# Kernel optimization log

Measured on AMD Instinct MI355X. Metric: run time of the kernel, lower is better.

## Reference

```python
import jax, jax.numpy as jnp
import numpy as np

B, N, H, L, E, OUT = 32, 128, 128, 3, 65536, 128
AV, BV = 128, 16  # atom / bond feature vocab sizes
NEG = -1e9


def setup_inputs() -> dict:
    key = jax.random.key(0)
    ks = jax.random.split(key, 20)
    x = jax.random.randint(ks[0], (B * N, 9), 0, AV)          # OGB atom features
    edge_attr = jax.random.randint(ks[1], (E, 3), 0, BV)      # OGB bond features
    # within-graph random edges (PyG requires edges not to cross graphs)
    g = jax.random.randint(ks[2], (E,), 0, B)
    src = jax.random.randint(ks[3], (E,), 0, N)
    dst = jax.random.randint(ks[4], (E,), 0, N)
    edge_index = jnp.stack([g * N + src, g * N + dst])        # [2, E] global node ids
    batch_idx = jnp.repeat(jnp.arange(B), N)                  # equal-size graphs
    s = 0.05
    w = lambda k, *shape: jax.random.normal(k, shape, dtype=jnp.float32) * s
    return {
        "x": x, "edge_attr": edge_attr, "edge_index": edge_index, "batch_idx": batch_idx,
        "atom_emb": w(ks[5], 9, AV, H), "bond_emb": w(ks[6], 3, BV, H),
        "Wm1": w(ks[7], L, 2 * H, H), "bm1": jnp.zeros((L, H), jnp.float32),
        "Wm2": w(ks[8], L, 2 * H, H), "bm2": jnp.zeros((L, H), jnp.float32),
        "We": w(ks[9], L, H, H), "be": jnp.zeros((L, H), jnp.float32),
        "Wg": w(ks[10], L, H, H), "bg": jnp.zeros((L, H), jnp.float32),
        "Wp1": w(ks[11], L, H, H), "bp1": jnp.zeros((L, H), jnp.float32),
        "Wp2": w(ks[12], L, H, H), "bp2": jnp.zeros((L, H), jnp.float32),
        "Wo1": w(ks[13], L, 2 * H, H), "bo1": jnp.zeros((L, H), jnp.float32),
        "Wo2": w(ks[14], L, H, H), "bo2": jnp.zeros((L, H), jnp.float32),
        "ln_s": jnp.ones((L, H), jnp.float32), "ln_b": jnp.zeros((L, H), jnp.float32),
        "Wh1": w(ks[15], H, H), "bh1": jnp.zeros((H,), jnp.float32),
        "Wh2": w(ks[16], H, OUT), "bh2": jnp.zeros((OUT,), jnp.float32),
    }


def reference(x, edge_attr, edge_index, batch_idx, atom_emb, bond_emb,
              Wm1, bm1, Wm2, bm2, We, be, Wg, bg, Wp1, bp1, Wp2, bp2,
              Wo1, bo1, Wo2, bo2, ln_s, ln_b, Wh1, bh1, Wh2, bh2):
    # AtomEncoder / BondEncoder: sum of per-column embeddings
    node_fts = jnp.sum(atom_emb[jnp.arange(9), x], axis=1)        # [B*N, H]
    edge_fts = jnp.sum(bond_emb[jnp.arange(3), edge_attr], axis=1)  # [E, H]
    # to_dense_batch with equal-size graphs == reshape; mask all-True
    node_fts = node_fts.reshape(B, N, H)
    # to_dense_adj: scatter-add edge list into dense [B, N, N] (+features)
    g = edge_index[0] // N
    s_loc = edge_index[0] % N
    d_loc = edge_index[1] % N
    adj = jnp.zeros((B, N, N), jnp.float32).at[g, s_loc, d_loc].add(1.0)
    edge_dense = jnp.zeros((B, N, N, H), jnp.float32).at[g, s_loc, d_loc].add(edge_fts)
    graph_fts = jnp.zeros((B, H), jnp.float32)
    hidden = jnp.zeros_like(node_fts)
    adj_mask = (adj > 0)[..., None]                               # [B, Ns, Nr, 1]
    for l in range(L):  # CLRS-style MPNN layers
        z = jnp.concatenate([node_fts, hidden], axis=-1)          # [B, N, 2H]
        m1 = z @ Wm1[l] + bm1[l]
        m2 = z @ Wm2[l] + bm2[l]
        me = edge_dense @ We[l] + be[l]
        mg = graph_fts @ Wg[l] + bg[l]
        msgs = m1[:, :, None, :] + m2[:, None, :, :] + me + mg[:, None, None, :]
        msgs = jax.nn.relu(msgs)
        msgs = jax.nn.relu(msgs @ Wp1[l] + bp1[l]) @ Wp2[l] + bp2[l]  # msgs MLP [H,H]
        msgs = jnp.max(jnp.where(adj_mask, msgs, NEG), axis=1)   # masked max over senders
        h = jax.nn.relu(z @ Wo1[l] + bo1[l] + msgs @ Wo2[l] + bo2[l])
        mu = h.mean(-1, keepdims=True)
        var = ((h - mu) ** 2).mean(-1, keepdims=True)
        hidden = (h - mu) / jnp.sqrt(var + 1e-5) * ln_s[l] + ln_b[l]
    # masked mean pool (mask is all-True here) + prediction MLP
    graph_emb = hidden.mean(axis=1)                               # [B, H]
    return jax.nn.relu(graph_emb @ Wh1 + bh1) @ Wh2 + bh2         # [B, OUT]
```

## Files before the change

### kernel.cpp

```cpp
#include <hip/hip_runtime.h>
#include <hip/hip_bf16.h>

#define NB_ 32
#define LL_ 3
#define EE_ 65536
#define NODES_ 4096
#define SLOTS_ 524288
#define NEGV -1e9f

typedef _Float16 f16x8 __attribute__((ext_vector_type(8)));
typedef float f32x4 __attribute__((ext_vector_type(4)));

__device__ __forceinline__ unsigned fkey(float f) {
  unsigned b = __float_as_uint(f);
  unsigned m = ((int)b >> 31) | 0x80000000u;
  return b ^ m;
}
__device__ __forceinline__ float funkey(unsigned k) {
  unsigned xm = (k & 0x80000000u) ? 0x80000000u : 0xFFFFFFFFu;
  return __uint_as_float(k ^ xm);
}

__global__ __launch_bounds__(256) void k_pro(const int* __restrict__ x,
    const float* __restrict__ atom_emb, _Float16* __restrict__ zh,
    const float* __restrict__ Wp1, const float* __restrict__ Wp2,
    const float* __restrict__ Wm1, const float* __restrict__ Wm2,
    const float* __restrict__ Wo1, const float* __restrict__ Wo2,
    _Float16* __restrict__ Whf,
    const float* __restrict__ bond_emb, const float* __restrict__ We,
    _Float16* __restrict__ bembWeh,
    const int* __restrict__ ei, int* __restrict__ cnt, int* __restrict__ erank) {
  int blk = blockIdx.x, tid = threadIdx.x;
  if (blk < 2048) {
    int v = blk * 2 + (tid >> 7), t = tid & 127;
    float acc = 0.f;
#pragma unroll
    for (int c = 0; c < 9; c++) {
      int xv = x[v * 9 + c];
      acc += atom_emb[(c * 128 + xv) * 128 + t];
    }
    zh[v * 256 + t] = (_Float16)acc;
    zh[v * 256 + 128 + t] = (_Float16)0.f;
  } else if (blk < 2264) {
    int gid = (blk - 2048) * 256 + tid;
    int lane = gid & 63;
    int llo = lane & 15, lhi = lane >> 4;
    const float* W; int col, kbase;
    if (gid < 12288) {
      int mat = gid >> 11, pos = gid & 2047;
      int fr = pos >> 6; int ct = fr >> 2, kt = fr & 3;
      int lyr = mat >> 1, which = mat & 1;
      W = (which ? Wp2 : Wp1) + lyr * 16384;
      col = ct * 16 + llo; kbase = kt * 32 + lhi * 8;
    } else if (gid < 36864) {
      int q = gid - 12288;
      int lyr = q >> 13, r = q & 8191;
      int fr = r >> 6; int ct = fr >> 3, kt = fr & 7;
      col = ct * 16 + llo; kbase = kt * 32 + lhi * 8;
      if (col < 128) { W = Wm1 + lyr * 32768; }
      else { W = Wm2 + lyr * 32768; col -= 128; }
    } else {
      int q = gid - 36864;
      int lyr = q / 6144, r = q % 6144;
      int fr = r >> 6; int ct = fr / 12, kt = fr % 12;
      col = ct * 16 + llo; kbase = kt * 32 + lhi * 8;
      if (kbase < 256) { W = Wo1 + lyr * 32768; }
      else { W = Wo2 + lyr * 16384; kbase -= 256; }
    }
    f16x8 h;
#pragma unroll
    for (int e = 0; e < 8; e++) h[e] = (_Float16)W[(kbase + e) * 128 + col];
    ((f16x8*)Whf)[gid] = h;
  } else if (blk < 2336) {
    __shared__ float row[2][128];
    int rid = (blk - 2264) * 2 + (tid >> 7);
    int half = tid >> 7, c = tid & 127;
    int l = rid / 48, rr = rid % 48;
    row[half][c] = bond_emb[rr * 128 + c];
    __syncthreads();
    const float* W = We + l * 16384;
    float acc = 0.f;
    for (int k = 0; k < 128; k += 4) {
      acc += row[half][k] * W[k * 128 + c] +
             row[half][k + 1] * W[(k + 1) * 128 + c] +
             row[half][k + 2] * W[(k + 2) * 128 + c] +
             row[half][k + 3] * W[(k + 3) * 128 + c];
    }
    bembWeh[(l * 48 + rr) * 128 + c] = (_Float16)acc;
  } else {
    int e = (blk - 2336) * 256 + tid;
    int s = ei[e], d = ei[EE_ + e];
    int g = s >> 7, i = s & 127, j = d & 127;
    int slot = ((g << 7) + j) * 128 + i;
    erank[e] = atomicAdd(&cnt[slot], 1);
  }
}

__global__ __launch_bounds__(256) void k_scanA(const int* __restrict__ cnt,
    int* __restrict__ basep, int* __restrict__ pairbase,
    int* __restrict__ bsumA, int* __restrict__ bsumF) {
  __shared__ int sA[256], sF[256];
  int t = threadIdx.x, gid = blockIdx.x * 256 + t;
  int v = cnt[gid];
  int f = v > 0 ? 1 : 0;
  sA[t] = v; sF[t] = f; __syncthreads();
  for (int st = 1; st < 256; st <<= 1) {
    int aA = sA[t], aF = sF[t];
    int bA = (t >= st) ? sA[t - st] : 0;
    int bF = (t >= st) ? sF[t - st] : 0;
    __syncthreads();
    sA[t] = aA + bA; sF[t] = aF + bF;
    __syncthreads();
  }
  basep[gid] = sA[t] - v;
  pairbase[gid] = sF[t] - f;
  if (t == 255) { bsumA[blockIdx.x] = sA[255]; bsumF[blockIdx.x] = sF[255]; }
}

__global__ __launch_bounds__(256) void k_scan2d(int* __restrict__ bsumA,
                                                int* __restrict__ bsumF) {
  int* bsum = blockIdx.x ? bsumF : bsumA;
  __shared__ int s[256];
  int t = threadIdx.x;
  int v[8]; int tot = 0;
#pragma unroll
  for (int q = 0; q < 8; q++) { v[q] = bsum[t * 8 + q]; tot += v[q]; }
  s[t] = tot; __syncthreads();
  for (int st = 1; st < 256; st <<= 1) {
    int a = s[t]; int b = (t >= st) ? s[t - st] : 0;
    __syncthreads(); s[t] = a + b; __syncthreads();
  }
  int run = s[t] - tot;
#pragma unroll
  for (int q = 0; q < 8; q++) { int tmp = v[q]; bsum[t * 8 + q] = run; run += tmp; }
}

__global__ __launch_bounds__(256) void k_scanBS(const int* __restrict__ cnt,
    const int* __restrict__ basep, const int* __restrict__ pairbase,
    const int* __restrict__ bsumA, const int* __restrict__ bsumF,
    int* __restrict__ pair_total, int* __restrict__ pair_slot,
    int* __restrict__ pair_off, int* __restrict__ pair_cnt,
    const int* __restrict__ ei, const int* __restrict__ erank,
    int* __restrict__ sorted_e) {
  int blk = blockIdx.x, tid = threadIdx.x;
  if (blk < 2048) {
    int gid = blk * 256 + tid;
    int b = basep[gid] + bsumA[gid >> 8];
    int pb = pairbase[gid] + bsumF[gid >> 8];
    int c = cnt[gid];
    if (c > 0) {
      pair_slot[pb] = gid;
      pair_off[pb] = b;
      pair_cnt[pb] = c;
    }
    if (gid == SLOTS_ - 1) pair_total[0] = pb + (c > 0 ? 1 : 0);
  } else {
    int e = (blk - 2048) * 256 + tid;
    int s = ei[e], d = ei[EE_ + e];
    int g = s >> 7, i = s & 127, j = d & 127;
    int slot = ((g << 7) + j) * 128 + i;
    int pos = basep[slot] + bsumA[slot >> 8] + erank[e];
    sorted_e[pos] = e;
  }
}

__global__ __launch_bounds__(256, 4) void k_m12(const _Float16* __restrict__ zh,
    const _Float16* __restrict__ Whf, const float* __restrict__ bm1,
    const float* __restrict__ bm2, _Float16* __restrict__ mm,
    unsigned* __restrict__ msgs_u, int l) {
  int tid = threadIdx.x;
  {
    int g0 = blockIdx.x * 256 + tid;
    unsigned kneg = fkey(NEGV);
    msgs_u[g0] = kneg;
    msgs_u[g0 + 262144] = kneg;
  }
  int wv = tid >> 6, l64 = tid & 63;
  int llo = l64 & 15, lhi = l64 >> 4;
  int tile = blockIdx.x >> 2;
  int ct = (blockIdx.x & 3) * 4 + wv;
  int row = tile * 16 + llo;
  f16x8 a[8];
#pragma unroll
  for (int kt = 0; kt < 8; kt++)
    a[kt] = *(const f16x8*)(zh + row * 256 + kt * 32 + lhi * 8);
  const f16x8* Bf = (const f16x8*)Whf + 12288 + l * 8192;
  int col = ct * 16 + llo;
  float bv = (col < 128) ? bm1[l * 128 + col] : bm2[l * 128 + col - 128];
  f32x4 acc = {bv, bv, bv, bv};
#pragma unroll
  for (int kt = 0; kt < 8; kt++)
    acc = __builtin_amdgcn_mfma_f32_16x16x32_f16(a[kt], Bf[(ct * 8 + kt) * 64 + l64], acc, 0, 0, 0);
#pragma unroll
  for (int reg = 0; reg < 4; reg++)
    mm[(tile * 16 + lhi * 4 + reg) * 256 + col] = (_Float16)acc[reg];
}

__global__ __launch_bounds__(256, 4) void k_pairs(
    const _Float16* __restrict__ mm,
    const int* __restrict__ pair_slot, const int* __restrict__ pair_off,
    const int* __restrict__ pair_cnt, const int* __restrict__ pair_total,
    const int* __restrict__ sorted_e, const int* __restrict__ edge_attr,
    const _Float16* __restrict__ bembWeh,
    const float* __restrict__ be, const float* __restrict__ bg,
    const _Float16* __restrict__ Whf,
    const float* __restrict__ bp1, const float* __restrict__ bp2,
    unsigned* __restrict__ msgs_u, int l) {
  __shared__ int s_slot[64], s_off[64], s_cnt[64], s_lrow[64];
  __shared__ int s_scan[64];
  __shared__ int s_rid[16];
  __shared__ int s_nrecv;
  __shared__ unsigned Lmax[16 * 128];
  __shared__ _Float16 Uh[64 * 128];
  int P = pair_total[0];
  int pid0 = blockIdx.x * 64;
  if (pid0 >= P) return;
  int tid = threadIdx.x;
  {
    unsigned kneg = fkey(NEGV);
#pragma unroll
    for (int q = 0; q < 8; q++) Lmax[tid + q * 256] = kneg;
  }
  if (tid < 64) {
    int pid = pid0 + tid;
    bool va = pid < P;
    s_slot[tid] = va ? pair_slot[pid] : -1;
    s_off[tid] = va ? pair_off[pid] : 0;
    s_cnt[tid] = va ? pair_cnt[pid] : 0;
  }
  __syncthreads();
  if (tid < 64) {
    int slot = s_slot[tid];
    int r = slot >= 0 ? (slot >> 7) : -1;
    int pr = (tid == 0) ? -2 : (s_slot[tid - 1] >= 0 ? (s_slot[tid - 1] >> 7) : -1);
    s_scan[tid] = (slot >= 0 && r != pr) ? 1 : 0;
  }
  __syncthreads();
  for (int st = 1; st < 64; st <<= 1) {
    int a = 0, b = 0;
    if (tid < 64) { a = s_scan[tid]; b = (tid >= st) ? s_scan[tid - st] : 0; }
    __syncthreads();
    if (tid < 64) s_scan[tid] = a + b;
    __syncthreads();
  }
  if (tid < 64) {
    int slot = s_slot[tid];
    int lr = s_scan[tid] - 1;
    s_lrow[tid] = lr;
    int r = slot >= 0 ? (slot >> 7) : -1;
    int pr = (tid == 0) ? -2 : (s_slot[tid - 1] >= 0 ? (s_slot[tid - 1] >> 7) : -1);
    if (slot >= 0 && r != pr && lr < 16) s_rid[lr] = r;
    if (tid == 63) s_nrecv = s_scan[63];
  }
  __syncthreads();

  int l64 = tid & 63, wv = tid >> 6;
  int llo = l64 & 15, lhi = l64 >> 4;
  int p = wv * 16 + llo;
  int slot = s_slot[p];
  float t32[4][8];
  if (slot >= 0) {
    int rr = slot >> 7, i = slot & 127, g = slot >> 14;
    int sn = (g << 7) + i;
#pragma unroll
    for (int kt = 0; kt < 4; kt++) {
      int c0 = kt * 32 + lhi * 8;
      f16x8 v1 = *(const f16x8*)(mm + sn * 256 + c0);
      f16x8 v2 = *(const f16x8*)(mm + rr * 256 + 128 + c0);
      float4 e0 = *(const float4*)(be + l * 128 + c0);
      float4 e1 = *(const float4*)(be + l * 128 + c0 + 4);
      float4 g0 = *(const float4*)(bg + l * 128 + c0);
      float4 g1 = *(const float4*)(bg + l * 128 + c0 + 4);
      t32[kt][0] = (float)v1[0] + (float)v2[0] + e0.x + g0.x;
      t32[kt][1] = (float)v1[1] + (float)v2[1] + e0.y + g0.y;
      t32[kt][2] = (float)v1[2] + (float)v2[2] + e0.z + g0.z;
      t32[kt][3] = (float)v1[3] + (float)v2[3] + e0.w + g0.w;
      t32[kt][4] = (float)v1[4] + (float)v2[4] + e1.x + g1.x;
      t32[kt][5] = (float)v1[5] + (float)v2[5] + e1.y + g1.y;
      t32[kt][6] = (float)v1[6] + (float)v2[6] + e1.z + g1.z;
      t32[kt][7] = (float)v1[7] + (float)v2[7] + e1.w + g1.w;
    }
    int off = s_off[p], cn = s_cnt[p];
    for (int d = 0; d < cn; d++) {
      int eid = sorted_e[off + d];
      int a0 = edge_attr[eid * 3], a1 = edge_attr[eid * 3 + 1],
          a2 = edge_attr[eid * 3 + 2];
      const _Float16* r0 = bembWeh + (l * 48 + a0) * 128;
      const _Float16* r1 = bembWeh + (l * 48 + 16 + a1) * 128;
      const _Float16* r2 = bembWeh + (l * 48 + 32 + a2) * 128;
#pragma unroll
      for (int kt = 0; kt < 4; kt++) {
        int c0 = kt * 32 + lhi * 8;
        f16x8 x0 = *(const f16x8*)(r0 + c0);
        f16x8 x1 = *(const f16x8*)(r1 + c0);
        f16x8 x2 = *(const f16x8*)(r2 + c0);
#pragma unroll
        for (int e = 0; e < 8; e++)
          t32[kt][e] += (float)x0[e] + (float)x1[e] + (float)x2[e];
      }
    }
  } else {
#pragma unroll
    for (int kt = 0; kt < 4; kt++)
#pragma unroll
      for (int e = 0; e < 8; e++) t32[kt][e] = 0.f;
  }
  f16x8 a[4];
#pragma unroll
  for (int kt = 0; kt < 4; kt++)
#pragma unroll
    for (int e = 0; e < 8; e++) a[kt][e] = (_Float16)fmaxf(t32[kt][e], 0.f);

  const f16x8* W1f = (const f16x8*)Whf + (l * 2) * 2048;
  const f16x8* W2f = (const f16x8*)Whf + (l * 2 + 1) * 2048;
#pragma unroll
  for (int ct = 0; ct < 8; ct++) {
    int col = ct * 16 + llo;
    float b1 = bp1[l * 128 + col];
    f32x4 acc = {b1, b1, b1, b1};
#pragma unroll
    for (int kt = 0; kt < 4; kt++)
      acc = __builtin_amdgcn_mfma_f32_16x16x32_f16(a[kt], W1f[(ct * 4 + kt) * 64 + l64], acc, 0, 0, 0);
#pragma unroll
    for (int reg = 0; reg < 4; reg++) {
      int wrow = wv * 16 + lhi * 4 + reg;
      int sg = (2 * ct + (llo >> 3)) ^ (wrow & 15);
      Uh[wrow * 128 + sg * 8 + (llo & 7)] = (_Float16)fmaxf(acc[reg], 0.f);
    }
  }
  __syncthreads();
  f16x8 a2[4];
  int arow = wv * 16 + llo;
#pragma unroll
  for (int kt = 0; kt < 4; kt++) {
    int sg = (kt * 4 + lhi) ^ (arow & 15);
    a2[kt] = *(const f16x8*)(Uh + arow * 128 + sg * 8);
  }
#pragma unroll
  for (int ct = 0; ct < 8; ct++) {
    int col = ct * 16 + llo;
    float b2 = bp2[l * 128 + col];
    f32x4 acc = {b2, b2, b2, b2};
#pragma unroll
    for (int kt = 0; kt < 4; kt++)
      acc = __builtin_amdgcn_mfma_f32_16x16x32_f16(a2[kt], W2f[(ct * 4 + kt) * 64 + l64], acc, 0, 0, 0);
    int prev_lr = -2, prev_rr = -1; float run = 0.f;
#pragma unroll
    for (int reg = 0; reg < 4; reg++) {
      int prow = wv * 16 + lhi * 4 + reg;
      int slot2 = s_slot[prow];
      if (slot2 < 0) continue;
      int lr = s_lrow[prow];
      float v = acc[reg];
      if (lr == prev_lr) {
        run = fmaxf(run, v);
      } else {
        if (prev_lr >= 0) {
          if (prev_lr < 16) atomicMax(&Lmax[prev_lr * 128 + col], fkey(run));
          else atomicMax(&msgs_u[prev_rr * 128 + col], fkey(run));
        }
        prev_lr = lr; prev_rr = slot2 >> 7; run = v;
      }
    }
    if (prev_lr >= 0) {
      if (prev_lr < 16) atomicMax(&Lmax[prev_lr * 128 + col], fkey(run));
      else atomicMax(&msgs_u[prev_rr * 128 + col], fkey(run));
    }
  }
  __syncthreads();
  int nr = s_nrecv; if (nr > 16) nr = 16;
  for (int base = 0; base < nr; base += 2) {
    int lr = base + (tid >> 7);
    int col = tid & 127;
    if (lr < nr)
      atomicMax(&msgs_u[s_rid[lr] * 128 + col], Lmax[lr * 128 + col]);
  }
}

__global__ __launch_bounds__(512, 2) void k_out_ln(_Float16* __restrict__ zh,
    const unsigned* __restrict__ msgs_u, const _Float16* __restrict__ Whf,
    const float* __restrict__ bo1, const float* __restrict__ bo2,
    const float* __restrict__ ln_s, const float* __restrict__ ln_b, int l) {
  __shared__ float sumA[8][16];
  __shared__ float muS[16], rsS[16];
  int tid = threadIdx.x;
  int wv = tid >> 6, l64 = tid & 63;
  int llo = l64 & 15, lhi = l64 >> 4;
  int row = blockIdx.x * 16 + llo;
  f16x8 a[12];
#pragma unroll
  for (int kt = 0; kt < 8; kt++)
    a[kt] = *(const f16x8*)(zh + row * 256 + kt * 32 + lhi * 8);
#pragma unroll
  for (int kt = 8; kt < 12; kt++) {
    int k0 = (kt - 8) * 32 + lhi * 8;
    f16x8 h;
#pragma unroll
    for (int e = 0; e < 8; e++) {
      float v = funkey(msgs_u[row * 128 + k0 + e]);
      v = fmaxf(fminf(v, 60000.f), -60000.f);
      h[e] = (_Float16)v;
    }
    a[kt] = h;
  }
  const f16x8* Bf = (const f16x8*)Whf + 36864 + l * 6144;
  int ct = wv, col = ct * 16 + llo;
  float bv = bo1[l * 128 + col] + bo2[l * 128 + col];
  f32x4 acc = {bv, bv, bv, bv};
#pragma unroll
  for (int kt = 0; kt < 12; kt++)
    acc = __builtin_amdgcn_mfma_f32_16x16x32_f16(a[kt], Bf[(ct * 12 + kt) * 64 + l64], acc, 0, 0, 0);
  float h[4];
#pragma unroll
  for (int reg = 0; reg < 4; reg++) h[reg] = fmaxf(acc[reg], 0.f);
#pragma unroll
  for (int reg = 0; reg < 4; reg++) {
    float s = h[reg];
    s += __shfl_xor(s, 1, 64); s += __shfl_xor(s, 2, 64);
    s += __shfl_xor(s, 4, 64); s += __shfl_xor(s, 8, 64);
    if (llo == 0) sumA[wv][lhi * 4 + reg] = s;
  }
  __syncthreads();
  if (tid < 16) {
    float s = 0.f;
#pragma unroll
    for (int w = 0; w < 8; w++) s += sumA[w][tid];
    muS[tid] = s * (1.f / 128.f);
  }
  __syncthreads();
#pragma unroll
  for (int reg = 0; reg < 4; reg++) {
    float d = h[reg] - muS[lhi * 4 + reg];
    float s = d * d;
    s += __shfl_xor(s, 1, 64); s += __shfl_xor(s, 2, 64);
    s += __shfl_xor(s, 4, 64); s += __shfl_xor(s, 8, 64);
    if (llo == 0) sumA[wv][lhi * 4 + reg] = s;
  }
  __syncthreads();
  if (tid < 16) {
    float s = 0.f;
#pragma unroll
    for (int w = 0; w < 8; w++) s += sumA[w][tid];
    rsS[tid] = rsqrtf(s * (1.f / 128.f) + 1e-5f);
  }
  __syncthreads();
  float sc = ln_s[l * 128 + col], bb = ln_b[l * 128 + col];
#pragma unroll
  for (int reg = 0; reg < 4; reg++) {
    int rr = lhi * 4 + reg;
    int wrow = blockIdx.x * 16 + rr;
    zh[wrow * 256 + 128 + col] =
        (_Float16)((h[reg] - muS[rr]) * rsS[rr] * sc + bb);
  }
}

__global__ __launch_bounds__(128) void k_head(const _Float16* __restrict__ zh,
    const float* __restrict__ Wh1, const float* __restrict__ bh1,
    const float* __restrict__ Wh2, const float* __restrict__ bh2,
    float* __restrict__ out) {
  __shared__ float ge[128], p1[128];
  int b = blockIdx.x, t = threadIdx.x;
  float s = 0.f;
  for (int n = 0; n < 128; n++) s += (float)zh[(b * 128 + n) * 256 + 128 + t];
  ge[t] = s * (1.f / 128.f);
  __syncthreads();
  float a = bh1[t];
  for (int k = 0; k < 128; k++) a += ge[k] * Wh1[k * 128 + t];
  p1[t] = fmaxf(a, 0.f);
  __syncthreads();
  float o = bh2[t];
  for (int k = 0; k < 128; k++) o += p1[k] * Wh2[k * 128 + t];
  out[b * 128 + t] = o;
}

extern "C" void kernel_launch(void* const* d_in, const int* in_sizes, int n_in,
                              void* d_out, int out_size, void* d_ws, size_t ws_size,
                              hipStream_t stream) {
  const int* x          = (const int*)d_in[0];
  const int* edge_attr  = (const int*)d_in[1];
  const int* edge_index = (const int*)d_in[2];
  const float* atom_emb = (const float*)d_in[4];
  const float* bond_emb = (const float*)d_in[5];
  const float* Wm1 = (const float*)d_in[6];
  const float* bm1 = (const float*)d_in[7];
  const float* Wm2 = (const float*)d_in[8];
  const float* bm2 = (const float*)d_in[9];
  const float* We  = (const float*)d_in[10];
  const float* be  = (const float*)d_in[11];
  const float* bg  = (const float*)d_in[13];
  const float* Wp1 = (const float*)d_in[14];
  const float* bp1 = (const float*)d_in[15];
  const float* Wp2 = (const float*)d_in[16];
  const float* bp2 = (const float*)d_in[17];
  const float* Wo1 = (const float*)d_in[18];
  const float* bo1 = (const float*)d_in[19];
  const float* Wo2 = (const float*)d_in[20];
  const float* bo2 = (const float*)d_in[21];
  const float* ln_s = (const float*)d_in[22];
  const float* ln_b = (const float*)d_in[23];
  const float* Wh1 = (const float*)d_in[24];
  const float* bh1 = (const float*)d_in[25];
  const float* Wh2 = (const float*)d_in[26];
  const float* bh2 = (const float*)d_in[27];
  float* out = (float*)d_out;

  int* cnt       = (int*)d_ws;
  int* basep     = cnt + SLOTS_;
  int* pairbase  = basep + SLOTS_;
  int* bsumA     = pairbase + SLOTS_;
  int* bsumF     = bsumA + 2048;
  int* pair_tot  = bsumF + 2048;
  int* erank     = pair_tot + 16;
  int* sorted_e  = erank + EE_;
  int* pair_slot = sorted_e + EE_;
  int* pair_off  = pair_slot + EE_;
  int* pair_cnt  = pair_off + EE_;
  unsigned* msgs_u = (unsigned*)(pair_cnt + EE_);
  _Float16* zh   = (_Float16*)(msgs_u + SLOTS_);
  _Float16* mm   = zh + NODES_ * 256;
  _Float16* bembWeh = mm + NODES_ * 256;
  _Float16* Whf  = bembWeh + 3 * 48 * 128;

  hipMemsetAsync(cnt, 0, SLOTS_ * sizeof(int), stream);

  k_pro<<<2592, 256, 0, stream>>>(x, atom_emb, zh, Wp1, Wp2, Wm1, Wm2, Wo1, Wo2,
                                  Whf, bond_emb, We, bembWeh, edge_index, cnt,
                                  erank);
  k_scanA<<<SLOTS_ / 256, 256, 0, stream>>>(cnt, basep, pairbase, bsumA, bsumF);
  k_scan2d<<<2, 256, 0, stream>>>(bsumA, bsumF);
  k_scanBS<<<2304, 256, 0, stream>>>(cnt, basep, pairbase, bsumA, bsumF,
                                     pair_tot, pair_slot, pair_off, pair_cnt,
                                     edge_index, erank, sorted_e);

  for (int l = 0; l < LL_; l++) {
    k_m12<<<1024, 256, 0, stream>>>(zh, Whf, bm1, bm2, mm, msgs_u, l);
    k_pairs<<<1024, 256, 0, stream>>>(mm, pair_slot, pair_off, pair_cnt,
                                      pair_tot, sorted_e, edge_attr, bembWeh,
                                      be, bg, Whf, bp1, bp2, msgs_u, l);
    k_out_ln<<<NODES_ / 16, 512, 0, stream>>>(zh, msgs_u, Whf, bo1, bo2,
                                              ln_s, ln_b, l);
  }
  k_head<<<NB_, 128, 0, stream>>>(zh, Wh1, bh1, Wh2, bh2, out);
}
```

Before: 267.8 us.

## Precompute per-pair edge projections once and fuse out-LN with next layer m12

```diff
diff --git a/kernel.cpp b/kernel.cpp
--- a/kernel.cpp
+++ b/kernel.cpp
@@ -26,9 +26,7 @@
     const float* __restrict__ Wp1, const float* __restrict__ Wp2,
     const float* __restrict__ Wm1, const float* __restrict__ Wm2,
     const float* __restrict__ Wo1, const float* __restrict__ Wo2,
-    _Float16* __restrict__ Whf,
-    const float* __restrict__ bond_emb, const float* __restrict__ We,
-    _Float16* __restrict__ bembWeh,
+    const float* __restrict__ We, _Float16* __restrict__ Whf,
     const int* __restrict__ ei, int* __restrict__ cnt, int* __restrict__ erank) {
   int blk = blockIdx.x, tid = threadIdx.x;
   if (blk < 2048) {
@@ -41,7 +39,7 @@
     }
     zh[v * 256 + t] = (_Float16)acc;
     zh[v * 256 + 128 + t] = (_Float16)0.f;
-  } else if (blk < 2264) {
+  } else if (blk < 2288) {
     int gid = (blk - 2048) * 256 + tid;
     int lane = gid & 63;
     int llo = lane & 15, lhi = lane >> 4;
@@ -59,36 +57,26 @@
       col = ct * 16 + llo; kbase = kt * 32 + lhi * 8;
       if (col < 128) { W = Wm1 + lyr * 32768; }
       else { W = Wm2 + lyr * 32768; col -= 128; }
-    } else {
+    } else if (gid < 55296) {
       int q = gid - 36864;
       int lyr = q / 6144, r = q % 6144;
       int fr = r >> 6; int ct = fr / 12, kt = fr % 12;
       col = ct * 16 + llo; kbase = kt * 32 + lhi * 8;
       if (kbase < 256) { W = Wo1 + lyr * 32768; }
       else { W = Wo2 + lyr * 16384; kbase -= 256; }
+    } else {
+      int q = gid - 55296;
+      int lyr = q >> 11, r = q & 2047;
+      int fr = r >> 6; int ct = fr >> 2, kt = fr & 3;
+      W = We + lyr * 16384;
+      col = ct * 16 + llo; kbase = kt * 32 + lhi * 8;
     }
     f16x8 h;
 #pragma unroll
     for (int e = 0; e < 8; e++) h[e] = (_Float16)W[(kbase + e) * 128 + col];
     ((f16x8*)Whf)[gid] = h;
-  } else if (blk < 2336) {
-    __shared__ float row[2][128];
-    int rid = (blk - 2264) * 2 + (tid >> 7);
-    int half = tid >> 7, c = tid & 127;
-    int l = rid / 48, rr = rid % 48;
-    row[half][c] = bond_emb[rr * 128 + c];
-    __syncthreads();
-    const float* W = We + l * 16384;
-    float acc = 0.f;
-    for (int k = 0; k < 128; k += 4) {
-      acc += row[half][k] * W[k * 128 + c] +
-             row[half][k + 1] * W[(k + 1) * 128 + c] +
-             row[half][k + 2] * W[(k + 2) * 128 + c] +
-             row[half][k + 3] * W[(k + 3) * 128 + c];
-    }
-    bembWeh[(l * 48 + rr) * 128 + c] = (_Float16)acc;
   } else {
-    int e = (blk - 2336) * 256 + tid;
+    int e = (blk - 2288) * 256 + tid;
     int s = ei[e], d = ei[EE_ + e];
     int g = s >> 7, i = s & 127, j = d & 127;
     int slot = ((g << 7) + j) * 128 + i;
@@ -164,6 +152,74 @@
   }
 }
 
+__global__ __launch_bounds__(256, 4) void k_epre(
+    const int* __restrict__ pair_off, const int* __restrict__ pair_cnt,
+    const int* __restrict__ pair_total, const int* __restrict__ sorted_e,
+    const int* __restrict__ edge_attr, const float* __restrict__ bond_emb,
+    const _Float16* __restrict__ Whf, _Float16* __restrict__ eWeh) {
+  __shared__ int s_off[64], s_cnt[64];
+  int P = pair_total[0];
+  int pid0 = blockIdx.x * 64;
+  if (pid0 >= P) return;
+  int tid = threadIdx.x;
+  if (tid < 64) {
+    int pid = pid0 + tid;
+    bool va = pid < P;
+    s_off[tid] = va ? pair_off[pid] : 0;
+    s_cnt[tid] = va ? pair_cnt[pid] : 0;
+  }
+  __syncthreads();
+  int l64 = tid & 63, wv = tid >> 6;
+  int llo = l64 & 15, lhi = l64 >> 4;
+  int p = wv * 16 + llo;
+  float eb[4][8];
+#pragma unroll
+  for (int kt = 0; kt < 4; kt++)
+#pragma unroll
+    for (int e = 0; e < 8; e++) eb[kt][e] = 0.f;
+  int off = s_off[p], cn = s_cnt[p];
+  for (int d = 0; d < cn; d++) {
+    int eid = sorted_e[off + d];
+    int a0 = edge_attr[eid * 3], a1 = edge_attr[eid * 3 + 1],
+        a2 = edge_attr[eid * 3 + 2];
+    const float* r0 = bond_emb + a0 * 128;
+    const float* r1 = bond_emb + (16 + a1) * 128;
+    const float* r2 = bond_emb + (32 + a2) * 128;
+#pragma unroll
+    for (int kt = 0; kt < 4; kt++) {
+      int c0 = kt * 32 + lhi * 8;
+      float4 xa = *(const float4*)(r0 + c0), xb = *(const float4*)(r0 + c0 + 4);
+      float4 ya = *(const float4*)(r1 + c0), yb = *(const float4*)(r1 + c0 + 4);
+      float4 za = *(const float4*)(r2 + c0), zb = *(const float4*)(r2 + c0 + 4);
+      eb[kt][0] += xa.x + ya.x + za.x; eb[kt][1] += xa.y + ya.y + za.y;
+      eb[kt][2] += xa.z + ya.z + za.z; eb[kt][3] += xa.w + ya.w + za.w;
+      eb[kt][4] += xb.x + yb.x + zb.x; eb[kt][5] += xb.y + yb.y + zb.y;
+      eb[kt][6] += xb.z + yb.z + zb.z; eb[kt][7] += xb.w + yb.w + zb.w;
+    }
+  }
+  f16x8 a[4];
+#pragma unroll
+  for (int kt = 0; kt < 4; kt++)
+#pragma unroll
+    for (int e = 0; e < 8; e++) a[kt][e] = (_Float16)eb[kt][e];
+#pragma unroll
+  for (int l = 0; l < LL_; l++) {
+    const f16x8* WeF = (const f16x8*)Whf + 55296 + l * 2048;
+#pragma unroll
+    for (int ct = 0; ct < 8; ct++) {
+      f32x4 acc = {0.f, 0.f, 0.f, 0.f};
+#pragma unroll
+      for (int kt = 0; kt < 4; kt++)
+        acc = __builtin_amdgcn_mfma_f32_16x16x32_f16(a[kt], WeF[(ct * 4 + kt) * 64 + l64], acc, 0, 0, 0);
+#pragma unroll
+      for (int reg = 0; reg < 4; reg++) {
+        int pw = wv * 16 + lhi * 4 + reg;
+        eWeh[((size_t)l * EE_ + pid0 + pw) * 128 + ct * 16 + llo] = (_Float16)acc[reg];
+      }
+    }
+  }
+}
+
 __global__ __launch_bounds__(256, 4) void k_m12(const _Float16* __restrict__ zh,
     const _Float16* __restrict__ Whf, const float* __restrict__ bm1,
     const float* __restrict__ bm2, _Float16* __restrict__ mm,
@@ -198,15 +254,13 @@
 
 __global__ __launch_bounds__(256, 4) void k_pairs(
     const _Float16* __restrict__ mm,
-    const int* __restrict__ pair_slot, const int* __restrict__ pair_off,
-    const int* __restrict__ pair_cnt, const int* __restrict__ pair_total,
-    const int* __restrict__ sorted_e, const int* __restrict__ edge_attr,
-    const _Float16* __restrict__ bembWeh,
+    const int* __restrict__ pair_slot, const int* __restrict__ pair_total,
+    const _Float16* __restrict__ eWeh,
     const float* __restrict__ be, const float* __restrict__ bg,
     const _Float16* __restrict__ Whf,
     const float* __restrict__ bp1, const float* __restrict__ bp2,
     unsigned* __restrict__ msgs_u, int l) {
-  __shared__ int s_slot[64], s_off[64], s_cnt[64], s_lrow[64];
+  __shared__ int s_slot[64], s_lrow[64];
   __shared__ int s_scan[64];
   __shared__ int s_rid[16];
   __shared__ int s_nrecv;
@@ -223,10 +277,7 @@
   }
   if (tid < 64) {
     int pid = pid0 + tid;
-    bool va = pid < P;
-    s_slot[tid] = va ? pair_slot[pid] : -1;
-    s_off[tid] = va ? pair_off[pid] : 0;
-    s_cnt[tid] = va ? pair_cnt[pid] : 0;
+    s_slot[tid] = (pid < P) ? pair_slot[pid] : -1;
   }
   __syncthreads();
   if (tid < 64) {
@@ -258,58 +309,41 @@
   int llo = l64 & 15, lhi = l64 >> 4;
   int p = wv * 16 + llo;
   int slot = s_slot[p];
-  float t32[4][8];
+  f16x8 a[4];
   if (slot >= 0) {
     int rr = slot >> 7, i = slot & 127, g = slot >> 14;
     int sn = (g << 7) + i;
+    int pid = pid0 + p;
+    const _Float16* ewp = eWeh + ((size_t)l * EE_ + pid) * 128;
 #pragma unroll
     for (int kt = 0; kt < 4; kt++) {
       int c0 = kt * 32 + lhi * 8;
       f16x8 v1 = *(const f16x8*)(mm + sn * 256 + c0);
       f16x8 v2 = *(const f16x8*)(mm + rr * 256 + 128 + c0);
+      f16x8 ew = *(const f16x8*)(ewp + c0);
       float4 e0 = *(const float4*)(be + l * 128 + c0);
       float4 e1 = *(const float4*)(be + l * 128 + c0 + 4);
       float4 g0 = *(const float4*)(bg + l * 128 + c0);
       float4 g1 = *(const float4*)(bg + l * 128 + c0 + 4);
-      t32[kt][0] = (float)v1[0] + (float)v2[0] + e0.x + g0.x;
-      t32[kt][1] = (float)v1[1] + (float)v2[1] + e0.y + g0.y;
-      t32[kt][2] = (float)v1[2] + (float)v2[2] + e0.z + g0.z;
-      t32[kt][3] = (float)v1[3] + (float)v2[3] + e0.w + g0.w;
-      t32[kt][4] = (float)v1[4] + (float)v2[4] + e1.x + g1.x;
-      t32[kt][5] = (float)v1[5] + (float)v2[5] + e1.y + g1.y;
-      t32[kt][6] = (float)v1[6] + (float)v2[6] + e1.z + g1.z;
-      t32[kt][7] = (float)v1[7] + (float)v2[7] + e1.w + g1.w;
-    }
-    int off = s_off[p], cn = s_cnt[p];
-    for (int d = 0; d < cn; d++) {
-      int eid = sorted_e[off + d];
-      int a0 = edge_attr[eid * 3], a1 = edge_attr[eid * 3 + 1],
-          a2 = edge_attr[eid * 3 + 2];
-      const _Float16* r0 = bembWeh + (l * 48 + a0) * 128;
-      const _Float16* r1 = bembWeh + (l * 48 + 16 + a1) * 128;
-      const _Float16* r2 = bembWeh + (l * 48 + 32 + a2) * 128;
-#pragma unroll
-      for (int kt = 0; kt < 4; kt++) {
-        int c0 = kt * 32 + lhi * 8;
-        f16x8 x0 = *(const f16x8*)(r0 + c0);
-        f16x8 x1 = *(const f16x8*)(r1 + c0);
-        f16x8 x2 = *(const f16x8*)(r2 + c0);
-#pragma unroll
-        for (int e = 0; e < 8; e++)
-          t32[kt][e] += (float)x0[e] + (float)x1[e] + (float)x2[e];
-      }
+      float t0 = (float)v1[0] + (float)v2[0] + (float)ew[0] + e0.x + g0.x;
+      float t1 = (float)v1[1] + (float)v2[1] + (float)ew[1] + e0.y + g0.y;
+      float t2 = (float)v1[2] + (float)v2[2] + (float)ew[2] + e0.z + g0.z;
+      float t3 = (float)v1[3] + (float)v2[3] + (float)ew[3] + e0.w + g0.w;
+      float t4 = (float)v1[4] + (float)v2[4] + (float)ew[4] + e1.x + g1.x;
+      float t5 = (float)v1[5] + (float)v2[5] + (float)ew[5] + e1.y + g1.y;
+      float t6 = (float)v1[6] + (float)v2[6] + (float)ew[6] + e1.z + g1.z;
+      float t7 = (float)v1[7] + (float)v2[7] + (float)ew[7] + e1.w + g1.w;
+      a[kt][0] = (_Float16)fmaxf(t0, 0.f); a[kt][1] = (_Float16)fmaxf(t1, 0.f);
+      a[kt][2] = (_Float16)fmaxf(t2, 0.f); a[kt][3] = (_Float16)fmaxf(t3, 0.f);
+      a[kt][4] = (_Float16)fmaxf(t4, 0.f); a[kt][5] = (_Float16)fmaxf(t5, 0.f);
+      a[kt][6] = (_Float16)fmaxf(t6, 0.f); a[kt][7] = (_Float16)fmaxf(t7, 0.f);
     }
   } else {
 #pragma unroll
     for (int kt = 0; kt < 4; kt++)
 #pragma unroll
-      for (int e = 0; e < 8; e++) t32[kt][e] = 0.f;
-  }
-  f16x8 a[4];
-#pragma unroll
-  for (int kt = 0; kt < 4; kt++)
-#pragma unroll
-    for (int e = 0; e < 8; e++) a[kt][e] = (_Float16)fmaxf(t32[kt][e], 0.f);
+      for (int e = 0; e < 8; e++) a[kt][e] = (_Float16)0.f;
+  }
 
   const f16x8* W1f = (const f16x8*)Whf + (l * 2) * 2048;
   const f16x8* W2f = (const f16x8*)Whf + (l * 2 + 1) * 2048;
@@ -374,6 +408,118 @@
     int col = tid & 127;
     if (lr < nr)
       atomicMax(&msgs_u[s_rid[lr] * 128 + col], Lmax[lr * 128 + col]);
+  }
+}
+
+__global__ __launch_bounds__(512, 2) void k_olnm12(_Float16* __restrict__ zh,
+    unsigned* __restrict__ msgs_u, const _Float16* __restrict__ Whf,
+    const float* __restrict__ bo1, const float* __restrict__ bo2,
+    const float* __restrict__ ln_s, const float* __restrict__ ln_b,
+    const float* __restrict__ bm1, const float* __restrict__ bm2,
+    _Float16* __restrict__ mm, int l) {
+  __shared__ float sumA[8][16];
+  __shared__ float muS[16], rsS[16];
+  __shared__ _Float16 hidT[16][132];
+  int tid = threadIdx.x;
+  int wv = tid >> 6, l64 = tid & 63;
+  int llo = l64 & 15, lhi = l64 >> 4;
+  int row = blockIdx.x * 16 + llo;
+  f16x8 a[12];
+#pragma unroll
+  for (int kt = 0; kt < 8; kt++)
+    a[kt] = *(const f16x8*)(zh + row * 256 + kt * 32 + lhi * 8);
+#pragma unroll
+  for (int kt = 8; kt < 12; kt++) {
+    int k0 = (kt - 8) * 32 + lhi * 8;
+    f16x8 h;
+#pragma unroll
+    for (int e = 0; e < 8; e++) {
+      float v = funkey(msgs_u[row * 128 + k0 + e]);
+      v = fmaxf(fminf(v, 60000.f), -60000.f);
+      h[e] = (_Float16)v;
+    }
+    a[kt] = h;
+  }
+  const f16x8* Bo = (const f16x8*)Whf + 36864 + l * 6144;
+  int ct = wv, col = ct * 16 + llo;
+  float bv = bo1[l * 128 + col] + bo2[l * 128 + col];
+  f32x4 acc = {bv, bv, bv, bv};
+#pragma unroll
+  for (int kt = 0; kt < 12; kt++)
+    acc = __builtin_amdgcn_mfma_f32_16x16x32_f16(a[kt], Bo[(ct * 12 + kt) * 64 + l64], acc, 0, 0, 0);
+  float h[4];
+#pragma unroll
+  for (int reg = 0; reg < 4; reg++) h[reg] = fmaxf(acc[reg], 0.f);
+#pragma unroll
+  for (int reg = 0; reg < 4; reg++) {
+    float s = h[reg];
+    s += __shfl_xor(s, 1, 64); s += __shfl_xor(s, 2, 64);
+    s += __shfl_xor(s, 4, 64); s += __shfl_xor(s, 8, 64);
+    if (llo == 0) sumA[wv][lhi * 4 + reg] = s;
+  }
+  __syncthreads();
+  if (tid < 16) {
+    float s = 0.f;
+#pragma unroll
+    for (int w = 0; w < 8; w++) s += sumA[w][tid];
+    muS[tid] = s * (1.f / 128.f);
+  }
+  __syncthreads();
+#pragma unroll
+  for (int reg = 0; reg < 4; reg++) {
+    float d = h[reg] - muS[lhi * 4 + reg];
+    float s = d * d;
+    s += __shfl_xor(s, 1, 64); s += __shfl_xor(s, 2, 64);
+    s += __shfl_xor(s, 4, 64); s += __shfl_xor(s, 8, 64);
+    if (llo == 0) sumA[wv][lhi * 4 + reg] = s;
+  }
+  __syncthreads();
+  if (tid < 16) {
+    float s = 0.f;
+#pragma unroll
+    for (int w = 0; w < 8; w++) s += sumA[w][tid];
+    rsS[tid] = rsqrtf(s * (1.f / 128.f) + 1e-5f);
+  }
+  __syncthreads();
+  float sc = ln_s[l * 128 + col], bb = ln_b[l * 128 + col];
+#pragma unroll
+  for (int reg = 0; reg < 4; reg++) {
+    int rr = lhi * 4 + reg;
+    int wrow = blockIdx.x * 16 + rr;
+    _Float16 hh = (_Float16)((h[reg] - muS[rr]) * rsS[rr] * sc + bb);
+    zh[wrow * 256 + 128 + col] = hh;
+    hidT[rr][col] = hh;
+  }
+  {
+    unsigned kneg = fkey(NEGV);
+    int base = blockIdx.x * 2048 + tid;
+    msgs_u[base] = kneg;
+    msgs_u[base + 512] = kneg;
+    msgs_u[base + 1024] = kneg;
+    msgs_u[base + 1536] = kneg;
+  }
+  __syncthreads();
+  f16x8 b[4];
+#pragma unroll
+  for (int kt = 0; kt < 4; kt++)
+    b[kt] = *(const f16x8*)(&hidT[llo][kt * 32 + lhi * 8]);
+  const f16x8* Bm = (const f16x8*)Whf + 12288 + (l + 1) * 8192;
+#pragma unroll
+  for (int q = 0; q < 2; q++) {
+    int ct2 = wv + q * 8;
+    int col2 = ct2 * 16 + llo;
+    float bv2 = (col2 < 128) ? bm1[(l + 1) * 128 + col2]
+                             : bm2[(l + 1) * 128 + col2 - 128];
+    f32x4 acc2 = {bv2, bv2, bv2, bv2};
+#pragma unroll
+    for (int kt = 0; kt < 4; kt++)
+      acc2 = __builtin_amdgcn_mfma_f32_16x16x32_f16(a[kt], Bm[(ct2 * 8 + kt) * 64 + l64], acc2, 0, 0, 0);
+#pragma unroll
+    for (int kt = 0; kt < 4; kt++)
+      acc2 = __builtin_amdgcn_mfma_f32_16x16x32_f16(b[kt], Bm[(ct2 * 8 + 4 + kt) * 64 + l64], acc2, 0, 0, 0);
+#pragma unroll
+    for (int reg = 0; reg < 4; reg++)
+      mm[(blockIdx.x * 16 + lhi * 4 + reg) * 256 + col2] = (_Float16)acc2[reg];
   }
 }
 
@@ -518,27 +664,33 @@
   unsigned* msgs_u = (unsigned*)(pair_cnt + EE_);
   _Float16* zh   = (_Float16*)(msgs_u + SLOTS_);
   _Float16* mm   = zh + NODES_ * 256;
-  _Float16* bembWeh = mm + NODES_ * 256;
-  _Float16* Whf  = bembWeh + 3 * 48 * 128;
+  _Float16* Whf  = mm + NODES_ * 256;
+  _Float16* eWeh = Whf + 61440 * 8;
 
   hipMemsetAsync(cnt, 0, SLOTS_ * sizeof(int), stream);
 
-  k_pro<<<2592, 256, 0, stream>>>(x, atom_emb, zh, Wp1, Wp2, Wm1, Wm2, Wo1, Wo2,
-                                  Whf, bond_emb, We, bembWeh, edge_index, cnt,
-                                  erank);
+  k_pro<<<2544, 256, 0, stream>>>(x, atom_emb, zh, Wp1, Wp2, Wm1, Wm2, Wo1, Wo2,
+                                  We, Whf, edge_index, cnt, erank);
   k_scanA<<<SLOTS_ / 256, 256, 0, stream>>>(cnt, basep, pairbase, bsumA, bsumF);
   k_scan2d<<<2, 256, 0, stream>>>(bsumA, bsumF);
   k_scanBS<<<2304, 256, 0, stream>>>(cnt, basep, pairbase, bsumA, bsumF,
                                      pair_tot, pair_slot, pair_off, pair_cnt,
                                      edge_index, erank, sorted_e);
-
-  for (int l = 0; l < LL_; l++) {
-    k_m12<<<1024, 256, 0, stream>>>(zh, Whf, bm1, bm2, mm, msgs_u, l);
-    k_pairs<<<1024, 256, 0, stream>>>(mm, pair_slot, pair_off, pair_cnt,
-                                      pair_tot, sorted_e, edge_attr, bembWeh,
-                                      be, bg, Whf, bp1, bp2, msgs_u, l);
-    k_out_ln<<<NODES_ / 16, 512, 0, stream>>>(zh, msgs_u, Whf, bo1, bo2,
-                                              ln_s, ln_b, l);
-  }
+  k_epre<<<1024, 256, 0, stream>>>(pair_off, pair_cnt, pair_tot, sorted_e,
+                                   edge_attr, bond_emb, Whf, eWeh);
+
+  k_m12<<<1024, 256, 0, stream>>>(zh, Whf, bm1, bm2, mm, msgs_u, 0);
+  k_pairs<<<1024, 256, 0, stream>>>(mm, pair_slot, pair_tot, eWeh, be, bg, Whf,
+                                    bp1, bp2, msgs_u, 0);
+  k_olnm12<<<NODES_ / 16, 512, 0, stream>>>(zh, msgs_u, Whf, bo1, bo2, ln_s,
+                                            ln_b, bm1, bm2, mm, 0);
+  k_pairs<<<1024, 256, 0, stream>>>(mm, pair_slot, pair_tot, eWeh, be, bg, Whf,
+                                    bp1, bp2, msgs_u, 1);
+  k_olnm12<<<NODES_ / 16, 512, 0, stream>>>(zh, msgs_u, Whf, bo1, bo2, ln_s,
+                                            ln_b, bm1, bm2, mm, 1);
+  k_pairs<<<1024, 256, 0, stream>>>(mm, pair_slot, pair_tot, eWeh, be, bg, Whf,
+                                    bp1, bp2, msgs_u, 2);
+  k_out_ln<<<NODES_ / 16, 512, 0, stream>>>(zh, msgs_u, Whf, bo1, bo2,
+                                            ln_s, ln_b, 2);
   k_head<<<NB_, 128, 0, stream>>>(zh, Wh1, bh1, Wh2, bh2, out);
 }
```

Result: slower. 275.7 us (+3.0%).

## Fuse output-LayerNorm with next layer's m1/m2 projection and msgs reset

Applied to the files above, without the earlier changes.

```diff
diff --git a/kernel.cpp b/kernel.cpp
--- a/kernel.cpp
+++ b/kernel.cpp
@@ -258,10 +258,11 @@
   int llo = l64 & 15, lhi = l64 >> 4;
   int p = wv * 16 + llo;
   int slot = s_slot[p];
-  float t32[4][8];
+  f16x8 a[4];
   if (slot >= 0) {
     int rr = slot >> 7, i = slot & 127, g = slot >> 14;
     int sn = (g << 7) + i;
+    float t32[4][8];
 #pragma unroll
     for (int kt = 0; kt < 4; kt++) {
       int c0 = kt * 32 + lhi * 8;
@@ -299,17 +300,16 @@
           t32[kt][e] += (float)x0[e] + (float)x1[e] + (float)x2[e];
       }
     }
+#pragma unroll
+    for (int kt = 0; kt < 4; kt++)
+#pragma unroll
+      for (int e = 0; e < 8; e++) a[kt][e] = (_Float16)fmaxf(t32[kt][e], 0.f);
   } else {
 #pragma unroll
     for (int kt = 0; kt < 4; kt++)
 #pragma unroll
-      for (int e = 0; e < 8; e++) t32[kt][e] = 0.f;
-  }
-  f16x8 a[4];
-#pragma unroll
-  for (int kt = 0; kt < 4; kt++)
-#pragma unroll
-    for (int e = 0; e < 8; e++) a[kt][e] = (_Float16)fmaxf(t32[kt][e], 0.f);
+      for (int e = 0; e < 8; e++) a[kt][e] = (_Float16)0.f;
+  }
 
   const f16x8* W1f = (const f16x8*)Whf + (l * 2) * 2048;
   const f16x8* W2f = (const f16x8*)Whf + (l * 2 + 1) * 2048;
@@ -374,6 +374,118 @@
     int col = tid & 127;
     if (lr < nr)
       atomicMax(&msgs_u[s_rid[lr] * 128 + col], Lmax[lr * 128 + col]);
+  }
+}
+
+__global__ __launch_bounds__(512, 2) void k_olnm12(_Float16* __restrict__ zh,
+    unsigned* __restrict__ msgs_u, const _Float16* __restrict__ Whf,
+    const float* __restrict__ bo1, const float* __restrict__ bo2,
+    const float* __restrict__ ln_s, const float* __restrict__ ln_b,
+    const float* __restrict__ bm1, const float* __restrict__ bm2,
+    _Float16* __restrict__ mm, int l) {
+  __shared__ float sumA[8][16];
+  __shared__ float muS[16], rsS[16];
+  __shared__ _Float16 hidT[16][132];
+  int tid = threadIdx.x;
+  int wv = tid >> 6, l64 = tid & 63;
+  int llo = l64 & 15, lhi = l64 >> 4;
+  int row = blockIdx.x * 16 + llo;
+  f16x8 a[12];
+#pragma unroll
+  for (int kt = 0; kt < 8; kt++)
+    a[kt] = *(const f16x8*)(zh + row * 256 + kt * 32 + lhi * 8);
+#pragma unroll
+  for (int kt = 8; kt < 12; kt++) {
+    int k0 = (kt - 8) * 32 + lhi * 8;
+    f16x8 h;
+#pragma unroll
+    for (int e = 0; e < 8; e++) {
+      float v = funkey(msgs_u[row * 128 + k0 + e]);
+      v = fmaxf(fminf(v, 60000.f), -60000.f);
+      h[e] = (_Float16)v;
+    }
+    a[kt] = h;
+  }
+  const f16x8* Bo = (const f16x8*)Whf + 36864 + l * 6144;
+  int ct = wv, col = ct * 16 + llo;
+  float bv = bo1[l * 128 + col] + bo2[l * 128 + col];
+  f32x4 acc = {bv, bv, bv, bv};
+#pragma unroll
+  for (int kt = 0; kt < 12; kt++)
+    acc = __builtin_amdgcn_mfma_f32_16x16x32_f16(a[kt], Bo[(ct * 12 + kt) * 64 + l64], acc, 0, 0, 0);
+  float h[4];
+#pragma unroll
+  for (int reg = 0; reg < 4; reg++) h[reg] = fmaxf(acc[reg], 0.f);
+#pragma unroll
+  for (int reg = 0; reg < 4; reg++) {
+    float s = h[reg];
+    s += __shfl_xor(s, 1, 64); s += __shfl_xor(s, 2, 64);
+    s += __shfl_xor(s, 4, 64); s += __shfl_xor(s, 8, 64);
+    if (llo == 0) sumA[wv][lhi * 4 + reg] = s;
+  }
+  __syncthreads();
+  if (tid < 16) {
+    float s = 0.f;
+#pragma unroll
+    for (int w = 0; w < 8; w++) s += sumA[w][tid];
+    muS[tid] = s * (1.f / 128.f);
+  }
+  __syncthreads();
+#pragma unroll
+  for (int reg = 0; reg < 4; reg++) {
+    float d = h[reg] - muS[lhi * 4 + reg];
+    float s = d * d;
+    s += __shfl_xor(s, 1, 64); s += __shfl_xor(s, 2, 64);
+    s += __shfl_xor(s, 4, 64); s += __shfl_xor(s, 8, 64);
+    if (llo == 0) sumA[wv][lhi * 4 + reg] = s;
+  }
+  __syncthreads();
+  if (tid < 16) {
+    float s = 0.f;
+#pragma unroll
+    for (int w = 0; w < 8; w++) s += sumA[w][tid];
+    rsS[tid] = rsqrtf(s * (1.f / 128.f) + 1e-5f);
+  }
+  __syncthreads();
+  float sc = ln_s[l * 128 + col], bb = ln_b[l * 128 + col];
+#pragma unroll
+  for (int reg = 0; reg < 4; reg++) {
+    int rr = lhi * 4 + reg;
+    int wrow = blockIdx.x * 16 + rr;
+    _Float16 hh = (_Float16)((h[reg] - muS[rr]) * rsS[rr] * sc + bb);
+    zh[wrow * 256 + 128 + col] = hh;
+    hidT[rr][col] = hh;
+  }
+  {
+    unsigned kneg = fkey(NEGV);
+    int base = blockIdx.x * 2048 + tid;
+    msgs_u[base] = kneg;
+    msgs_u[base + 512] = kneg;
+    msgs_u[base + 1024] = kneg;
+    msgs_u[base + 1536] = kneg;
+  }
+  __syncthreads();
+  f16x8 b[4];
+#pragma unroll
+  for (int kt = 0; kt < 4; kt++)
+    b[kt] = *(const f16x8*)(&hidT[llo][kt * 32 + lhi * 8]);
+  const f16x8* Bm = (const f16x8*)Whf + 12288 + (l + 1) * 8192;
+#pragma unroll
+  for (int q = 0; q < 2; q++) {
+    int ct2 = wv + q * 8;
+    int col2 = ct2 * 16 + llo;
+    float bv2 = (col2 < 128) ? bm1[(l + 1) * 128 + col2]
+                             : bm2[(l + 1) * 128 + col2 - 128];
+    f32x4 acc2 = {bv2, bv2, bv2, bv2};
+#pragma unroll
+    for (int kt = 0; kt < 4; kt++)
+      acc2 = __builtin_amdgcn_mfma_f32_16x16x32_f16(a[kt], Bm[(ct2 * 8 + kt) * 64 + l64], acc2, 0, 0, 0);
+#pragma unroll
+    for (int kt = 0; kt < 4; kt++)
+      acc2 = __builtin_amdgcn_mfma_f32_16x16x32_f16(b[kt], Bm[(ct2 * 8 + 4 + kt) * 64 + l64], acc2, 0, 0, 0);
+#pragma unroll
+    for (int reg = 0; reg < 4; reg++)
+      mm[(blockIdx.x * 16 + lhi * 4 + reg) * 256 + col2] = (_Float16)acc2[reg];
   }
 }
 
@@ -532,13 +644,21 @@
                                      pair_tot, pair_slot, pair_off, pair_cnt,
                                      edge_index, erank, sorted_e);
 
-  for (int l = 0; l < LL_; l++) {
-    k_m12<<<1024, 256, 0, stream>>>(zh, Whf, bm1, bm2, mm, msgs_u, l);
-    k_pairs<<<1024, 256, 0, stream>>>(mm, pair_slot, pair_off, pair_cnt,
-                                      pair_tot, sorted_e, edge_attr, bembWeh,
-                                      be, bg, Whf, bp1, bp2, msgs_u, l);
-    k_out_ln<<<NODES_ / 16, 512, 0, stream>>>(zh, msgs_u, Whf, bo1, bo2,
-                                              ln_s, ln_b, l);
-  }
+  k_m12<<<1024, 256, 0, stream>>>(zh, Whf, bm1, bm2, mm, msgs_u, 0);
+  k_pairs<<<1024, 256, 0, stream>>>(mm, pair_slot, pair_off, pair_cnt,
+                                    pair_tot, sorted_e, edge_attr, bembWeh,
+                                    be, bg, Whf, bp1, bp2, msgs_u, 0);
+  k_olnm12<<<NODES_ / 16, 512, 0, stream>>>(zh, msgs_u, Whf, bo1, bo2, ln_s,
+                                            ln_b, bm1, bm2, mm, 0);
+  k_pairs<<<1024, 256, 0, stream>>>(mm, pair_slot, pair_off, pair_cnt,
+                                    pair_tot, sorted_e, edge_attr, bembWeh,
+                                    be, bg, Whf, bp1, bp2, msgs_u, 1);
+  k_olnm12<<<NODES_ / 16, 512, 0, stream>>>(zh, msgs_u, Whf, bo1, bo2, ln_s,
+                                            ln_b, bm1, bm2, mm, 1);
+  k_pairs<<<1024, 256, 0, stream>>>(mm, pair_slot, pair_off, pair_cnt,
+                                    pair_tot, sorted_e, edge_attr, bembWeh,
+                                    be, bg, Whf, bp1, bp2, msgs_u, 2);
+  k_out_ln<<<NODES_ / 16, 512, 0, stream>>>(zh, msgs_u, Whf, bo1, bo2,
+                                            ln_s, ln_b, 2);
   k_head<<<NB_, 128, 0, stream>>>(zh, Wh1, bh1, Wh2, bh2, out);
 }
```

New measurement: 257.3 us. -3.9%, faster.
